# Kernel optimization log

Hardware: AMD Instinct MI355X
Metric: run time of the kernel (lower is better)

## Reference

```python
import jax, jax.numpy as jnp
import numpy as np

N_NODES = 100000
N_EDGES = 1600000
IN, HID, OUT = 32, 32, 16


def setup_inputs() -> dict:
    key = jax.random.key(0)
    ks = jax.random.split(key, 8)
    return {
        "features": jax.random.normal(ks[0], (N_NODES, IN), dtype=jnp.float32),
        "src": jax.random.randint(ks[1], (N_EDGES,), 0, N_NODES, dtype=jnp.int32),
        "dst": jax.random.randint(ks[2], (N_EDGES,), 0, N_NODES, dtype=jnp.int32),
        "edge_weight": jax.random.uniform(ks[3], (N_EDGES,), dtype=jnp.float32),
        "W1": jax.random.normal(ks[4], (IN, HID), dtype=jnp.float32) * 0.1,
        "b1": jnp.zeros((HID,), dtype=jnp.float32),
        "W2": jax.random.normal(ks[5], (HID, OUT), dtype=jnp.float32) * 0.1,
        "b2": jnp.zeros((OUT,), dtype=jnp.float32),
    }


def _graph_conv(h, W, b, src, dst, edge_weight, norm_src, norm_dst, n):
    # DGL GraphConv, norm='both', with edge_weight (u_mul_e aggregation)
    h = h * norm_src[:, None]          # out-degree^-0.5 on source side
    h = h @ W                          # dense transform (tiny GEMM)
    m = h[src] * edge_weight[:, None]  # gather + edge weighting  [E, d]
    agg = jax.ops.segment_sum(m, dst, num_segments=n)  # scatter-add SpMM
    return agg * norm_dst[:, None] + b # in-degree^-0.5 + bias


def reference(features, src, dst, edge_weight, W1, b1, W2, b2):
    n = features.shape[0]
    ones_e = jnp.ones_like(edge_weight)
    deg_out = jnp.clip(jax.ops.segment_sum(ones_e, src, num_segments=n), 1.0)
    deg_in = jnp.clip(jax.ops.segment_sum(ones_e, dst, num_segments=n), 1.0)
    norm_src = deg_out ** -0.5
    norm_dst = deg_in ** -0.5
    h = _graph_conv(features, W1, b1, src, dst, edge_weight, norm_src, norm_dst, n)
    h = jax.nn.relu(h)
    # dropout is identity in eval mode
    h = _graph_conv(h, W2, b2, src, dst, edge_weight, norm_src, norm_dst, n)
    return h
```

## Files before the change

### kernel.cpp

```cpp
#include <hip/hip_runtime.h>
#include <hip/hip_fp16.h>


#define NB   391
#define CAPB 5504
#define EPB  4096

__device__ __forceinline__ long nt_load_i64(const long* p) {
    return __builtin_nontemporal_load(p);
}

__global__ __launch_bounds__(1024) void partition_kernel(
        const int* __restrict__ src, const int* __restrict__ dst,
        const float* __restrict__ ew,
        int* __restrict__ g_cur_d, int* __restrict__ g_cur_s,
        int2* __restrict__ pack_part, unsigned char* __restrict__ src_part, int m) {
    __shared__ int hist_d[NB], hist_s[NB];
    __shared__ int lbase_d[NB], lbase_s[NB];
    __shared__ int gbase_d[NB], gbase_s[NB];
    __shared__ int cur_d[NB], cur_s[NB];
    __shared__ int woffd[16], woffs[16];
    __shared__ long stage[EPB];
    __shared__ unsigned short dbuck[EPB];
    __shared__ unsigned char  sstage[EPB];
    __shared__ unsigned short sbuck[EPB];
    int t = threadIdx.x, lane = t & 63, w = t >> 6;
    for (int i = t; i < NB; i += 1024) {
        hist_d[i] = 0; hist_s[i] = 0; cur_d[i] = 0; cur_s[i] = 0;
    }
    __syncthreads();
    int base_e = blockIdx.x * EPB;
    int total = m - base_e; if (total > EPB) total = EPB;
    int es[4], ed[4]; float wv[4];
#pragma unroll
    for (int k = 0; k < 4; k++) {
        int e = base_e + k * 1024 + t;
        if (e < m) { es[k] = src[e]; ed[k] = dst[e]; wv[k] = ew[e]; }
        else ed[k] = -1;
    }
#pragma unroll
    for (int k = 0; k < 4; k++) {
        if (ed[k] >= 0) {
            atomicAdd(&hist_d[ed[k] >> 8], 1);
            atomicAdd(&hist_s[es[k] >> 8], 1);
        }
    }
    __syncthreads();
    int hvd = (t < NB) ? hist_d[t] : 0;
    int hvs = (t < NB) ? hist_s[t] : 0;
    int vd = hvd, vs = hvs;
#pragma unroll
    for (int off = 1; off < 64; off <<= 1) {
        int ud = __shfl_up(vd, off, 64);
        int us = __shfl_up(vs, off, 64);
        if (lane >= off) { vd += ud; vs += us; }
    }
    if (lane == 63) { woffd[w] = vd; woffs[w] = vs; }
    __syncthreads();
    if (t < 64) {
        int sd = (t < 16) ? woffd[t] : 0;
        int ss = (t < 16) ? woffs[t] : 0;
        int od = sd, os = ss;
#pragma unroll
        for (int off = 1; off < 16; off <<= 1) {
            int ud = __shfl_up(sd, off, 64);
            int us = __shfl_up(ss, off, 64);
            if (lane >= off) { sd += ud; ss += us; }
        }
        if (t < 16) { woffd[t] = sd - od; woffs[t] = ss - os; }
    }
    __syncthreads();
    if (t < NB) {
        lbase_d[t] = vd + woffd[w] - hvd;
        lbase_s[t] = vs + woffs[w] - hvs;
    }
    for (int i = t; i < NB; i += 1024) {
        int c = hist_d[i];
        gbase_d[i] = i * CAPB + (c ? atomicAdd(&g_cur_d[i], c) : 0);
        c = hist_s[i];
        gbase_s[i] = i * CAPB + (c ? atomicAdd(&g_cur_s[i], c) : 0);
    }
    __syncthreads();
#pragma unroll
    for (int k = 0; k < 4; k++) {
        if (ed[k] >= 0) {
            int d = ed[k], s = es[k];
            int bd = d >> 8;
            int r = atomicAdd(&cur_d[bd], 1);
            int pos = lbase_d[bd] + r;
            stage[pos] = (long)(unsigned int)(s | ((d & 255) << 20)) |
                         ((long)__float_as_int(wv[k]) << 32);
            dbuck[pos] = (unsigned short)bd;
            int bs = s >> 8;
            int rs = atomicAdd(&cur_s[bs], 1);
            int ps = lbase_s[bs] + rs;
            sstage[ps] = (unsigned char)(s & 255);
            sbuck[ps] = (unsigned short)bs;
        }
    }
    __syncthreads();
    long* packl = (long*)pack_part;
    for (int i = t; i < total; i += 1024) {
        int b = dbuck[i];
        packl[(size_t)gbase_d[b] + (i - lbase_d[b])] = stage[i];
    }
    for (int i = t; i < total; i += 1024) {
        int b = sbuck[i];
        src_part[(size_t)gbase_s[b] + (i - lbase_s[b])] = sstage[i];
    }
}

__global__ __launch_bounds__(1024) void csr_kernel(
                           const int2* __restrict__ pack_part,
                           const unsigned char* __restrict__ src_part,
                           const int* __restrict__ g_cur_d, const int* __restrict__ g_cur_s,
                           const float* __restrict__ feat, const float* __restrict__ W1,
                           int2* __restrict__ csr, int2* __restrict__ rs_cnt,
                           float* __restrict__ norm_src, float* __restrict__ norm_dst,
                           __half* __restrict__ h1, int n) {
    __shared__ int cnt[256];
    __shared__ int rowx[256];
    __shared__ int cur[256];
    __shared__ int cnt_s[256];
    __shared__ float nsrc[256];
    __shared__ float sW1[1024];
    extern __shared__ int2 stage[];
    int t = threadIdx.x, b = blockIdx.x;
    if (t < 256) { cnt[t] = 0; cur[t] = 0; cnt_s[t] = 0; }
    sW1[t] = W1[t];
    __syncthreads();
    int count = g_cur_d[b]; if (count > CAPB) count = CAPB;
    int count_s = g_cur_s[b]; if (count_s > CAPB) count_s = CAPB;
    const int2* p = pack_part + (size_t)b * CAPB;
    const unsigned char* sp = src_part + (size_t)b * CAPB;
    int2 pk[4];
#pragma unroll
    for (int u = 0; u < 4; u++) {
        int e = t + u * 1024;
        if (e < count) { pk[u] = p[e]; atomicAdd(&cnt[pk[u].x >> 20], 1); }
    }
    for (int e = t + 4096; e < count; e += 1024)
        atomicAdd(&cnt[p[e].x >> 20], 1);
    for (int e = t; e < count_s; e += 1024) atomicAdd(&cnt_s[sp[e]], 1);
    __syncthreads();
    if (t < 256) {
        int node = b * 256 + t;
        if (node < n) {
            int cs = cnt_s[t];
            float ns = rsqrtf((float)(cs > 1 ? cs : 1));
            nsrc[t] = ns;
            norm_src[node] = ns;
        } else nsrc[t] = 0.0f;
    }
    if (t < 64) {
        int c0 = cnt[t * 4], c1 = cnt[t * 4 + 1], c2 = cnt[t * 4 + 2], c3 = cnt[t * 4 + 3];
        int tot = c0 + c1 + c2 + c3;
        int incl = tot;
#pragma unroll
        for (int off = 1; off < 64; off <<= 1) {
            int u = __shfl_up(incl, off, 64);
            if (t >= off) incl += u;
        }
        int excl = incl - tot;
        rowx[t * 4]     = excl;
        rowx[t * 4 + 1] = excl + c0;
        rowx[t * 4 + 2] = excl + c0 + c1;
        rowx[t * 4 + 3] = excl + c0 + c1 + c2;
    }
    __syncthreads();
    if (t < 256) {
        int node = b * 256 + t;
        if (node < n) {
            rs_cnt[node] = make_int2(b * CAPB + rowx[t], cnt[t]);
            norm_dst[node] = rsqrtf((float)(cnt[t] > 1 ? cnt[t] : 1));
        }
    }
    __syncthreads();
#pragma unroll
    for (int u = 0; u < 4; u++) {
        int e = t + u * 1024;
        if (e < count) {
            int2 v = pk[u];
            int dl = v.x >> 20;
            int r = atomicAdd(&cur[dl], 1);
            stage[rowx[dl] + r] = make_int2(v.x & 0x1FFFF, v.y);
        }
    }
    for (int e = t + 4096; e < count; e += 1024) {
        int2 v = p[e];
        int dl = v.x >> 20;
        int r = atomicAdd(&cur[dl], 1);
        stage[rowx[dl] + r] = make_int2(v.x & 0x1FFFF, v.y);
    }
    __syncthreads();
    int2* outp = csr + (size_t)b * CAPB;
    for (int e = t; e < count; e += 1024) outp[e] = stage[e];
    __syncthreads();
    float* sF = (float*)stage;
    int node0 = b * 256;
    int lim = n - node0; if (lim > 256) lim = 256; if (lim < 0) lim = 0;
    for (int o = t; o < lim * 32; o += 1024) {
        int i = o >> 5, k = o & 31;
        sF[o] = feat[(size_t)(node0 + i) * 32 + k] * nsrc[i];
    }
    __syncthreads();
    for (int o = t; o < lim * 32; o += 1024) {
        int i = o >> 5, col = o & 31;
        float acc = 0.0f;
#pragma unroll
        for (int k = 0; k < 32; k++) acc += sF[i * 32 + k] * sW1[k * 32 + col];
        h1[(size_t)(node0 + i) * 32 + col] = __float2half(acc);
    }
}

__global__ void gather1_fused_kernel(const __half* __restrict__ h1, const int2* __restrict__ csr,
                                     const int2* __restrict__ rs_cnt,
                                     const float* __restrict__ norm_src, const float* __restrict__ norm_dst,
                                     const float* __restrict__ W2, const float* __restrict__ b1,
                                     __half* __restrict__ h2, int n) {
    __shared__ float sW2[32 * 16];
    __shared__ float sB1[32];
    __shared__ float sX[4][8][33];
    int t = threadIdx.x;
    for (int i = t; i < 512; i += 256) sW2[i] = W2[i];
    if (t < 32) sB1[t] = b1[t];
    __syncthreads();
    int w = t >> 6, lane = t & 63;
    int q = lane >> 3;
    int dq = lane & 7;
    int node = (blockIdx.x * 4 + w) * 8 + q;
    bool valid = node < n;
    int2 rc = valid ? rs_cnt[node] : make_int2(0, 0);
    long base = rc.x;
    int c = rc.y;
    const float2* tv = (const float2*)h1;
    const long* csrl = (const long*)csr;
    float a00=0,a01=0,a02=0,a03=0, a10=0,a11=0,a12=0,a13=0;
    float a20=0,a21=0,a22=0,a23=0, a30=0,a31=0,a32=0,a33=0;
    int j = 0;
    for (; j + 3 < c; j += 4) {
        long q0 = nt_load_i64(csrl + base + j);
        long q1 = nt_load_i64(csrl + base + j + 1);
        long q2 = nt_load_i64(csrl + base + j + 2);
        long q3 = nt_load_i64(csrl + base + j + 3);
        float2 r0 = tv[(size_t)((int)q0 & 0xFFFFF) * 8 + dq];
        float2 r1 = tv[(size_t)((int)q1 & 0xFFFFF) * 8 + dq];
        float2 r2 = tv[(size_t)((int)q2 & 0xFFFFF) * 8 + dq];
        float2 r3 = tv[(size_t)((int)q3 & 0xFFFFF) * 8 + dq];
        float w0 = __int_as_float((int)(q0 >> 32)), w1 = __int_as_float((int)(q1 >> 32));
        float w2 = __int_as_float((int)(q2 >> 32)), w3 = __int_as_float((int)(q3 >> 32));
        float2 l0 = __half22float2(*(__half2*)&r0.x), h0 = __half22float2(*(__half2*)&r0.y);
        float2 l1 = __half22float2(*(__half2*)&r1.x), h1v = __half22float2(*(__half2*)&r1.y);
        float2 l2 = __half22float2(*(__half2*)&r2.x), h2v = __half22float2(*(__half2*)&r2.y);
        float2 l3 = __half22float2(*(__half2*)&r3.x), h3v = __half22float2(*(__half2*)&r3.y);
        a00 += l0.x * w0; a01 += l0.y * w0; a02 += h0.x * w0; a03 += h0.y * w0;
        a10 += l1.x * w1; a11 += l1.y * w1; a12 += h1v.x * w1; a13 += h1v.y * w1;
        a20 += l2.x * w2; a21 += l2.y * w2; a22 += h2v.x * w2; a23 += h2v.y * w2;
        a30 += l3.x * w3; a31 += l3.y * w3; a32 += h3v.x * w3; a33 += h3v.y * w3;
    }
    for (; j < c; j++) {
        long qq = nt_load_i64(csrl + base + j);
        float2 r = tv[(size_t)((int)qq & 0xFFFFF) * 8 + dq];
        float ww = __int_as_float((int)(qq >> 32));
        float2 l = __half22float2(*(__half2*)&r.x), h = __half22float2(*(__half2*)&r.y);
        a00 += l.x * ww; a01 += l.y * ww; a02 += h.x * ww; a03 += h.y * ww;
    }
    float s0 = (a00 + a10) + (a20 + a30);
    float s1 = (a01 + a11) + (a21 + a31);
    float s2 = (a02 + a12) + (a22 + a32);
    float s3 = (a03 + a13) + (a23 + a33);
    if (valid) {
        float nd = norm_dst[node], ns = norm_src[node];
        int d0 = 4 * dq;
        sX[w][q][d0]     = fmaxf(s0 * nd + sB1[d0],     0.0f) * ns;
        sX[w][q][d0 + 1] = fmaxf(s1 * nd + sB1[d0 + 1], 0.0f) * ns;
        sX[w][q][d0 + 2] = fmaxf(s2 * nd + sB1[d0 + 2], 0.0f) * ns;
        sX[w][q][d0 + 3] = fmaxf(s3 * nd + sB1[d0 + 3], 0.0f) * ns;
    }
    if (valid) {
        float o0 = 0.0f, o1 = 0.0f;
        int c0 = 2 * dq, c1 = 2 * dq + 1;
#pragma unroll
        for (int k = 0; k < 32; k++) {
            float x = sX[w][q][k];
            o0 += x * sW2[k * 16 + c0];
            o1 += x * sW2[k * 16 + c1];
        }
        ((__half2*)h2)[(size_t)node * 8 + dq] = __floats2half2_rn(o0, o1);
    }
}

__global__ void gather2_kernel(const __half* __restrict__ h2, const int2* __restrict__ csr,
                               const int2* __restrict__ rs_cnt,
                               const float* __restrict__ norm_dst, const float* __restrict__ b2,
                               float* __restrict__ out, int n) {
    int t = threadIdx.x;
    int w = t >> 6, lane = t & 63;
    int q = lane >> 2;
    int dq = lane & 3;
    int node = (blockIdx.x * 4 + w) * 16 + q;
    bool valid = node < n;
    int2 rc = valid ? rs_cnt[node] : make_int2(0, 0);
    long base = rc.x;
    int c = rc.y;
    const float2* tv = (const float2*)h2;
    const long* csrl = (const long*)csr;
    float a00=0,a01=0,a02=0,a03=0, a10=0,a11=0,a12=0,a13=0;
    float a20=0,a21=0,a22=0,a23=0, a30=0,a31=0,a32=0,a33=0;
    int j = 0;
    for (; j + 3 < c; j += 4) {
        long q0 = nt_load_i64(csrl + base + j);
        long q1 = nt_load_i64(csrl + base + j + 1);
        long q2 = nt_load_i64(csrl + base + j + 2);
        long q3 = nt_load_i64(csrl + base + j + 3);
        float2 r0 = tv[(size_t)((int)q0 & 0xFFFFF) * 4 + dq];
        float2 r1 = tv[(size_t)((int)q1 & 0xFFFFF) * 4 + dq];
        float2 r2 = tv[(size_t)((int)q2 & 0xFFFFF) * 4 + dq];
        float2 r3 = tv[(size_t)((int)q3 & 0xFFFFF) * 4 + dq];
        float w0 = __int_as_float((int)(q0 >> 32)), w1 = __int_as_float((int)(q1 >> 32));
        float w2 = __int_as_float((int)(q2 >> 32)), w3 = __int_as_float((int)(q3 >> 32));
        float2 l0 = __half22float2(*(__half2*)&r0.x), h0 = __half22float2(*(__half2*)&r0.y);
        float2 l1 = __half22float2(*(__half2*)&r1.x), h1v = __half22float2(*(__half2*)&r1.y);
        float2 l2 = __half22float2(*(__half2*)&r2.x), h2v = __half22float2(*(__half2*)&r2.y);
        float2 l3 = __half22float2(*(__half2*)&r3.x), h3v = __half22float2(*(__half2*)&r3.y);
        a00 += l0.x * w0; a01 += l0.y * w0; a02 += h0.x * w0; a03 += h0.y * w0;
        a10 += l1.x * w1; a11 += l1.y * w1; a12 += h1v.x * w1; a13 += h1v.y * w1;
        a20 += l2.x * w2; a21 += l2.y * w2; a22 += h2v.x * w2; a23 += h2v.y * w2;
        a30 += l3.x * w3; a31 += l3.y * w3; a32 += h3v.x * w3; a33 += h3v.y * w3;
    }
    for (; j < c; j++) {
        long qq = nt_load_i64(csrl + base + j);
        float2 r = tv[(size_t)((int)qq & 0xFFFFF) * 4 + dq];
        float ww = __int_as_float((int)(qq >> 32));
        float2 l = __half22float2(*(__half2*)&r.x), h = __half22float2(*(__half2*)&r.y);
        a00 += l.x * ww; a01 += l.y * ww; a02 += h.x * ww; a03 += h.y * ww;
    }
    if (valid) {
        float nd = norm_dst[node];
        int d0 = 4 * dq;
        float4 o;
        o.x = ((a00 + a10) + (a20 + a30)) * nd + b2[d0];
        o.y = ((a01 + a11) + (a21 + a31)) * nd + b2[d0 + 1];
        o.z = ((a02 + a12) + (a22 + a32)) * nd + b2[d0 + 2];
        o.w = ((a03 + a13) + (a23 + a33)) * nd + b2[d0 + 3];
        ((float4*)out)[(size_t)node * 4 + dq] = o;
    }
}

extern "C" void kernel_launch(void* const* d_in, const int* in_sizes, int n_in,
                              void* d_out, int out_size, void* d_ws, size_t ws_size,
                              hipStream_t stream) {
    const float* feat = (const float*)d_in[0];
    const int*   src  = (const int*)d_in[1];
    const int*   dst  = (const int*)d_in[2];
    const float* ew   = (const float*)d_in[3];
    const float* W1   = (const float*)d_in[4];
    const float* b1   = (const float*)d_in[5];
    const float* W2   = (const float*)d_in[6];
    const float* b2   = (const float*)d_in[7];
    float* out = (float*)d_out;

    const int n = in_sizes[0] / 32;
    const int m = in_sizes[1];

    char* wsb = (char*)d_ws;
    int2*   pack_part = (int2*)wsb;
    int2*   csr       = pack_part + (size_t)NB * CAPB;
    __half* h1        = (__half*)(csr + (size_t)NB * CAPB);
    __half* h2        = h1 + 32 * (size_t)n;
    float*  norm_src  = (float*)(h2 + 16 * (size_t)n);
    float*  norm_dst  = norm_src + n;
    int2*   rs_cnt    = (int2*)(norm_dst + n);
    int*    g_cur_d   = (int*)(rs_cnt + n);
    int*    g_cur_s   = g_cur_d + NB;
    unsigned char* src_part = (unsigned char*)(g_cur_s + NB);

    hipMemsetAsync(g_cur_d, 0, 2 * NB * sizeof(int), stream);

    partition_kernel<<<(m + EPB - 1) / EPB, 1024, 0, stream>>>(src, dst, ew, g_cur_d, g_cur_s,
                                                               pack_part, src_part, m);
    csr_kernel<<<NB, 1024, CAPB * sizeof(int2), stream>>>(pack_part, src_part, g_cur_d, g_cur_s,
                                                          feat, W1, csr, rs_cnt,
                                                          norm_src, norm_dst, h1, n);
    gather1_fused_kernel<<<(n + 31) / 32, 256, 0, stream>>>(h1, csr, rs_cnt,
                                                            norm_src, norm_dst, W2, b1, h2, n);
    gather2_kernel<<<(n + 63) / 64, 256, 0, stream>>>(h2, csr, rs_cnt, norm_dst, b2, out, n);
}
```

Before: 186.8 us.

## Sub-sort CSR rows by source range to improve gather locality

The CSR build now buckets each destination row's edges into four sub-buckets keyed on the source node's high bits. This uses a 1024-entry histogram and scan instead of 256. Per-node sub-counts are stored so the first gather kernel walks the four source-range segments in order, aiming for better cache locality on the h1 feature gathers. It costs more shared-memory atomics and scan work in csr_kernel, plus an extra per-node ushort4 array and shorter inner loops with more tail iterations in gather1.

```diff
diff --git a/kernel.cpp b/kernel.cpp
--- a/kernel.cpp
+++ b/kernel.cpp
@@ -116,17 +116,19 @@
                            const int* __restrict__ g_cur_d, const int* __restrict__ g_cur_s,
                            const float* __restrict__ feat, const float* __restrict__ W1,
                            int2* __restrict__ csr, int2* __restrict__ rs_cnt,
+                           ushort4* __restrict__ subcnt,
                            float* __restrict__ norm_src, float* __restrict__ norm_dst,
                            __half* __restrict__ h1, int n) {
-    __shared__ int cnt[256];
-    __shared__ int rowx[256];
-    __shared__ int cur[256];
+    __shared__ int cnt4[1024];
+    __shared__ int rowx4[1024];
+    __shared__ int cur4[1024];
     __shared__ int cnt_s[256];
     __shared__ float nsrc[256];
     __shared__ float sW1[1024];
     extern __shared__ int2 stage[];
     int t = threadIdx.x, b = blockIdx.x;
-    if (t < 256) { cnt[t] = 0; cur[t] = 0; cnt_s[t] = 0; }
+    cnt4[t] = 0; cur4[t] = 0;
+    if (t < 256) cnt_s[t] = 0;
     sW1[t] = W1[t];
     __syncthreads();
     int count = g_cur_d[b]; if (count > CAPB) count = CAPB;
@@ -137,10 +139,16 @@
 #pragma unroll
     for (int u = 0; u < 4; u++) {
         int e = t + u * 1024;
-        if (e < count) { pk[u] = p[e]; atomicAdd(&cnt[pk[u].x >> 20], 1); }
-    }
-    for (int e = t + 4096; e < count; e += 1024)
-        atomicAdd(&cnt[p[e].x >> 20], 1);
+        if (e < count) {
+            pk[u] = p[e];
+            int key = ((pk[u].x >> 20) << 2) | ((pk[u].x & 0x1FFFF) >> 15);
+            atomicAdd(&cnt4[key], 1);
+        }
+    }
+    for (int e = t + 4096; e < count; e += 1024) {
+        int2 v = p[e];
+        atomicAdd(&cnt4[((v.x >> 20) << 2) | ((v.x & 0x1FFFF) >> 15)], 1);
+    }
     for (int e = t; e < count_s; e += 1024) atomicAdd(&cnt_s[sp[e]], 1);
     __syncthreads();
     if (t < 256) {
@@ -153,26 +161,30 @@
         } else nsrc[t] = 0.0f;
     }
     if (t < 64) {
-        int c0 = cnt[t * 4], c1 = cnt[t * 4 + 1], c2 = cnt[t * 4 + 2], c3 = cnt[t * 4 + 3];
-        int tot = c0 + c1 + c2 + c3;
-        int incl = tot;
+        int base16 = t * 16;
+        int loc[16]; int sum = 0;
+#pragma unroll
+        for (int i = 0; i < 16; i++) { loc[i] = cnt4[base16 + i]; sum += loc[i]; }
+        int incl = sum;
 #pragma unroll
         for (int off = 1; off < 64; off <<= 1) {
             int u = __shfl_up(incl, off, 64);
             if (t >= off) incl += u;
         }
-        int excl = incl - tot;
-        rowx[t * 4]     = excl;
-        rowx[t * 4 + 1] = excl + c0;
-        rowx[t * 4 + 2] = excl + c0 + c1;
-        rowx[t * 4 + 3] = excl + c0 + c1 + c2;
+        int run = incl - sum;
+#pragma unroll
+        for (int i = 0; i < 16; i++) { rowx4[base16 + i] = run; run += loc[i]; }
     }
     __syncthreads();
     if (t < 256) {
+        int c0 = cnt4[4 * t], c1 = cnt4[4 * t + 1], c2 = cnt4[4 * t + 2], c3 = cnt4[4 * t + 3];
+        int tot = c0 + c1 + c2 + c3;
         int node = b * 256 + t;
         if (node < n) {
-            rs_cnt[node] = make_int2(b * CAPB + rowx[t], cnt[t]);
-            norm_dst[node] = rsqrtf((float)(cnt[t] > 1 ? cnt[t] : 1));
+            rs_cnt[node] = make_int2(b * CAPB + rowx4[4 * t], tot);
+            norm_dst[node] = rsqrtf((float)(tot > 1 ? tot : 1));
+            subcnt[node] = make_ushort4((unsigned short)c0, (unsigned short)c1,
+                                        (unsigned short)c2, (unsigned short)c3);
         }
     }
     __syncthreads();
@@ -181,16 +193,16 @@
         int e = t + u * 1024;
         if (e < count) {
             int2 v = pk[u];
-            int dl = v.x >> 20;
-            int r = atomicAdd(&cur[dl], 1);
-            stage[rowx[dl] + r] = make_int2(v.x & 0x1FFFF, v.y);
+            int key = ((v.x >> 20) << 2) | ((v.x & 0x1FFFF) >> 15);
+            int r = atomicAdd(&cur4[key], 1);
+            stage[rowx4[key] + r] = make_int2(v.x & 0x1FFFF, v.y);
         }
     }
     for (int e = t + 4096; e < count; e += 1024) {
         int2 v = p[e];
-        int dl = v.x >> 20;
-        int r = atomicAdd(&cur[dl], 1);
-        stage[rowx[dl] + r] = make_int2(v.x & 0x1FFFF, v.y);
+        int key = ((v.x >> 20) << 2) | ((v.x & 0x1FFFF) >> 15);
+        int r = atomicAdd(&cur4[key], 1);
+        stage[rowx4[key] + r] = make_int2(v.x & 0x1FFFF, v.y);
     }
     __syncthreads();
     int2* outp = csr + (size_t)b * CAPB;
@@ -215,6 +227,7 @@
 
 __global__ void gather1_fused_kernel(const __half* __restrict__ h1, const int2* __restrict__ csr,
                                      const int2* __restrict__ rs_cnt,
+                                     const ushort4* __restrict__ subcnt,
                                      const float* __restrict__ norm_src, const float* __restrict__ norm_dst,
                                      const float* __restrict__ W2, const float* __restrict__ b1,
                                      __half* __restrict__ h2, int n) {
@@ -231,39 +244,45 @@
     int node = (blockIdx.x * 4 + w) * 8 + q;
     bool valid = node < n;
     int2 rc = valid ? rs_cnt[node] : make_int2(0, 0);
-    long base = rc.x;
-    int c = rc.y;
+    ushort4 sc = valid ? subcnt[node] : make_ushort4(0, 0, 0, 0);
     const float2* tv = (const float2*)h1;
     const long* csrl = (const long*)csr;
     float a00=0,a01=0,a02=0,a03=0, a10=0,a11=0,a12=0,a13=0;
     float a20=0,a21=0,a22=0,a23=0, a30=0,a31=0,a32=0,a33=0;
-    int j = 0;
-    for (; j + 3 < c; j += 4) {
-        long q0 = nt_load_i64(csrl + base + j);
-        long q1 = nt_load_i64(csrl + base + j + 1);
-        long q2 = nt_load_i64(csrl + base + j + 2);
-        long q3 = nt_load_i64(csrl + base + j + 3);
-        float2 r0 = tv[(size_t)((int)q0 & 0xFFFFF) * 8 + dq];
-        float2 r1 = tv[(size_t)((int)q1 & 0xFFFFF) * 8 + dq];
-        float2 r2 = tv[(size_t)((int)q2 & 0xFFFFF) * 8 + dq];
-        float2 r3 = tv[(size_t)((int)q3 & 0xFFFFF) * 8 + dq];
-        float w0 = __int_as_float((int)(q0 >> 32)), w1 = __int_as_float((int)(q1 >> 32));
-        float w2 = __int_as_float((int)(q2 >> 32)), w3 = __int_as_float((int)(q3 >> 32));
-        float2 l0 = __half22float2(*(__half2*)&r0.x), h0 = __half22float2(*(__half2*)&r0.y);
-        float2 l1 = __half22float2(*(__half2*)&r1.x), h1v = __half22float2(*(__half2*)&r1.y);
-        float2 l2 = __half22float2(*(__half2*)&r2.x), h2v = __half22float2(*(__half2*)&r2.y);
-        float2 l3 = __half22float2(*(__half2*)&r3.x), h3v = __half22float2(*(__half2*)&r3.y);
-        a00 += l0.x * w0; a01 += l0.y * w0; a02 += h0.x * w0; a03 += h0.y * w0;
-        a10 += l1.x * w1; a11 += l1.y * w1; a12 += h1v.x * w1; a13 += h1v.y * w1;
-        a20 += l2.x * w2; a21 += l2.y * w2; a22 += h2v.x * w2; a23 += h2v.y * w2;
-        a30 += l3.x * w3; a31 += l3.y * w3; a32 += h3v.x * w3; a33 += h3v.y * w3;
-    }
-    for (; j < c; j++) {
-        long qq = nt_load_i64(csrl + base + j);
-        float2 r = tv[(size_t)((int)qq & 0xFFFFF) * 8 + dq];
-        float ww = __int_as_float((int)(qq >> 32));
-        float2 l = __half22float2(*(__half2*)&r.x), h = __half22float2(*(__half2*)&r.y);
-        a00 += l.x * ww; a01 += l.y * ww; a02 += h.x * ww; a03 += h.y * ww;
+    int st = rc.x;
+#pragma unroll
+    for (int rr = 0; rr < 4; rr++) {
+        int c = (rr == 0) ? (int)sc.x : (rr == 1) ? (int)sc.y
+              : (rr == 2) ? (int)sc.z : (int)sc.w;
+        long base = st; st += c;
+        int j = 0;
+        for (; j + 3 < c; j += 4) {
+            long q0 = nt_load_i64(csrl + base + j);
+            long q1 = nt_load_i64(csrl + base + j + 1);
+            long q2 = nt_load_i64(csrl + base + j + 2);
+            long q3 = nt_load_i64(csrl + base + j + 3);
+            float2 r0 = tv[(size_t)((int)q0 & 0xFFFFF) * 8 + dq];
+            float2 r1 = tv[(size_t)((int)q1 & 0xFFFFF) * 8 + dq];
+            float2 r2 = tv[(size_t)((int)q2 & 0xFFFFF) * 8 + dq];
+            float2 r3 = tv[(size_t)((int)q3 & 0xFFFFF) * 8 + dq];
+            float w0 = __int_as_float((int)(q0 >> 32)), w1 = __int_as_float((int)(q1 >> 32));
+            float w2 = __int_as_float((int)(q2 >> 32)), w3 = __int_as_float((int)(q3 >> 32));
+            float2 l0 = __half22float2(*(__half2*)&r0.x), h0 = __half22float2(*(__half2*)&r0.y);
+            float2 l1 = __half22float2(*(__half2*)&r1.x), h1v = __half22float2(*(__half2*)&r1.y);
+            float2 l2 = __half22float2(*(__half2*)&r2.x), h2v = __half22float2(*(__half2*)&r2.y);
+            float2 l3 = __half22float2(*(__half2*)&r3.x), h3v = __half22float2(*(__half2*)&r3.y);
+            a00 += l0.x * w0; a01 += l0.y * w0; a02 += h0.x * w0; a03 += h0.y * w0;
+            a10 += l1.x * w1; a11 += l1.y * w1; a12 += h1v.x * w1; a13 += h1v.y * w1;
+            a20 += l2.x * w2; a21 += l2.y * w2; a22 += h2v.x * w2; a23 += h2v.y * w2;
+            a30 += l3.x * w3; a31 += l3.y * w3; a32 += h3v.x * w3; a33 += h3v.y * w3;
+        }
+        for (; j < c; j++) {
+            long qq = nt_load_i64(csrl + base + j);
+            float2 r = tv[(size_t)((int)qq & 0xFFFFF) * 8 + dq];
+            float ww = __int_as_float((int)(qq >> 32));
+            float2 l = __half22float2(*(__half2*)&r.x), h = __half22float2(*(__half2*)&r.y);
+            a00 += l.x * ww; a01 += l.y * ww; a02 += h.x * ww; a03 += h.y * ww;
+        }
     }
     float s0 = (a00 + a10) + (a20 + a30);
     float s1 = (a01 + a11) + (a21 + a31);
@@ -364,15 +383,16 @@
     const int m = in_sizes[1];
 
     char* wsb = (char*)d_ws;
-    int2*   pack_part = (int2*)wsb;
-    int2*   csr       = pack_part + (size_t)NB * CAPB;
-    __half* h1        = (__half*)(csr + (size_t)NB * CAPB);
-    __half* h2        = h1 + 32 * (size_t)n;
-    float*  norm_src  = (float*)(h2 + 16 * (size_t)n);
-    float*  norm_dst  = norm_src + n;
-    int2*   rs_cnt    = (int2*)(norm_dst + n);
-    int*    g_cur_d   = (int*)(rs_cnt + n);
-    int*    g_cur_s   = g_cur_d + NB;
+    int2*    pack_part = (int2*)wsb;
+    int2*    csr       = pack_part + (size_t)NB * CAPB;
+    __half*  h1        = (__half*)(csr + (size_t)NB * CAPB);
+    __half*  h2        = h1 + 32 * (size_t)n;
+    float*   norm_src  = (float*)(h2 + 16 * (size_t)n);
+    float*   norm_dst  = norm_src + n;
+    int2*    rs_cnt    = (int2*)(norm_dst + n);
+    ushort4* subcnt    = (ushort4*)(rs_cnt + n);
+    int*     g_cur_d   = (int*)(subcnt + n);
+    int*     g_cur_s   = g_cur_d + NB;
     unsigned char* src_part = (unsigned char*)(g_cur_s + NB);
 
     hipMemsetAsync(g_cur_d, 0, 2 * NB * sizeof(int), stream);
@@ -380,9 +400,9 @@
     partition_kernel<<<(m + EPB - 1) / EPB, 1024, 0, stream>>>(src, dst, ew, g_cur_d, g_cur_s,
                                                                pack_part, src_part, m);
     csr_kernel<<<NB, 1024, CAPB * sizeof(int2), stream>>>(pack_part, src_part, g_cur_d, g_cur_s,
-                                                          feat, W1, csr, rs_cnt,
+                                                          feat, W1, csr, rs_cnt, subcnt,
                                                           norm_src, norm_dst, h1, n);
-    gather1_fused_kernel<<<(n + 31) / 32, 256, 0, stream>>>(h1, csr, rs_cnt,
+    gather1_fused_kernel<<<(n + 31) / 32, 256, 0, stream>>>(h1, csr, rs_cnt, subcnt,
                                                             norm_src, norm_dst, W2, b1, h2, n);
     gather2_kernel<<<(n + 63) / 64, 256, 0, stream>>>(h2, csr, rs_cnt, norm_dst, b2, out, n);
 }
```

Result: slower. 194.4 us (+4.0%).

## Split first-layer gather into two feature-half passes to shrink gather footprint

Applied to the files above, without the earlier changes.

The 32-wide half-precision layer-1 features are stored as two separate 16-column arrays, and the layer-1 gather runs as two passes, one per half. Each pass does a partial second-layer GEMM. Pass 0 writes fp32 partials to a scratch buffer and pass 1 adds them and emits h2. The aim is to halve the random-gather working set per pass so it fits better in cache, at the cost of reading the CSR twice, an extra launch, and extra partial-sum traffic.

```diff
diff --git a/kernel.cpp b/kernel.cpp
--- a/kernel.cpp
+++ b/kernel.cpp
@@ -5,6 +5,8 @@
 #define NB   391
 #define CAPB 5504
 #define EPB  4096
+
+typedef float f32x4 __attribute__((ext_vector_type(4)));
 
 __device__ __forceinline__ long nt_load_i64(const long* p) {
     return __builtin_nontemporal_load(p);
@@ -117,7 +119,7 @@
                            const float* __restrict__ feat, const float* __restrict__ W1,
                            int2* __restrict__ csr, int2* __restrict__ rs_cnt,
                            float* __restrict__ norm_src, float* __restrict__ norm_dst,
-                           __half* __restrict__ h1, int n) {
+                           __half* __restrict__ h1a, __half* __restrict__ h1b, int n) {
     __shared__ int cnt[256];
     __shared__ int rowx[256];
     __shared__ int cur[256];
@@ -209,31 +211,34 @@
         float acc = 0.0f;
 #pragma unroll
         for (int k = 0; k < 32; k++) acc += sF[i * 32 + k] * sW1[k * 32 + col];
-        h1[(size_t)(node0 + i) * 32 + col] = __float2half(acc);
-    }
-}
-
-__global__ void gather1_fused_kernel(const __half* __restrict__ h1, const int2* __restrict__ csr,
-                                     const int2* __restrict__ rs_cnt,
-                                     const float* __restrict__ norm_src, const float* __restrict__ norm_dst,
-                                     const float* __restrict__ W2, const float* __restrict__ b1,
-                                     __half* __restrict__ h2, int n) {
-    __shared__ float sW2[32 * 16];
-    __shared__ float sB1[32];
-    __shared__ float sX[4][8][33];
+        __half hv = __float2half(acc);
+        if (col < 16) h1a[(size_t)(node0 + i) * 16 + col]        = hv;
+        else          h1b[(size_t)(node0 + i) * 16 + (col - 16)] = hv;
+    }
+}
+
+template<int PASS>
+__global__ void gather1_pass(const __half* __restrict__ h1x, const int2* __restrict__ csr,
+                             const int2* __restrict__ rs_cnt,
+                             const float* __restrict__ norm_src, const float* __restrict__ norm_dst,
+                             const float* __restrict__ W2, const float* __restrict__ b1,
+                             float* __restrict__ part, __half* __restrict__ h2, int n) {
+    __shared__ float sW2h[256];
+    __shared__ float sB[16];
+    __shared__ float sX[4][16][17];
     int t = threadIdx.x;
-    for (int i = t; i < 512; i += 256) sW2[i] = W2[i];
-    if (t < 32) sB1[t] = b1[t];
+    if (t < 256) sW2h[t] = W2[PASS * 256 + t];
+    if (t < 16)  sB[t] = b1[PASS * 16 + t];
     __syncthreads();
     int w = t >> 6, lane = t & 63;
-    int q = lane >> 3;
-    int dq = lane & 7;
-    int node = (blockIdx.x * 4 + w) * 8 + q;
+    int q = lane >> 2;
+    int dq = lane & 3;
+    int node = (blockIdx.x * 4 + w) * 16 + q;
     bool valid = node < n;
     int2 rc = valid ? rs_cnt[node] : make_int2(0, 0);
     long base = rc.x;
     int c = rc.y;
-    const float2* tv = (const float2*)h1;
+    const float2* tv = (const float2*)h1x;
     const long* csrl = (const long*)csr;
     float a00=0,a01=0,a02=0,a03=0, a10=0,a11=0,a12=0,a13=0;
     float a20=0,a21=0,a22=0,a23=0, a30=0,a31=0,a32=0,a33=0;
@@ -243,10 +248,10 @@
         long q1 = nt_load_i64(csrl + base + j + 1);
         long q2 = nt_load_i64(csrl + base + j + 2);
         long q3 = nt_load_i64(csrl + base + j + 3);
-        float2 r0 = tv[(size_t)((int)q0 & 0xFFFFF) * 8 + dq];
-        float2 r1 = tv[(size_t)((int)q1 & 0xFFFFF) * 8 + dq];
-        float2 r2 = tv[(size_t)((int)q2 & 0xFFFFF) * 8 + dq];
-        float2 r3 = tv[(size_t)((int)q3 & 0xFFFFF) * 8 + dq];
+        float2 r0 = tv[(size_t)((int)q0 & 0xFFFFF) * 4 + dq];
+        float2 r1 = tv[(size_t)((int)q1 & 0xFFFFF) * 4 + dq];
+        float2 r2 = tv[(size_t)((int)q2 & 0xFFFFF) * 4 + dq];
+        float2 r3 = tv[(size_t)((int)q3 & 0xFFFFF) * 4 + dq];
         float w0 = __int_as_float((int)(q0 >> 32)), w1 = __int_as_float((int)(q1 >> 32));
         float w2 = __int_as_float((int)(q2 >> 32)), w3 = __int_as_float((int)(q3 >> 32));
         float2 l0 = __half22float2(*(__half2*)&r0.x), h0 = __half22float2(*(__half2*)&r0.y);
@@ -260,7 +265,7 @@
     }
     for (; j < c; j++) {
         long qq = nt_load_i64(csrl + base + j);
-        float2 r = tv[(size_t)((int)qq & 0xFFFFF) * 8 + dq];
+        float2 r = tv[(size_t)((int)qq & 0xFFFFF) * 4 + dq];
         float ww = __int_as_float((int)(qq >> 32));
         float2 l = __half22float2(*(__half2*)&r.x), h = __half22float2(*(__half2*)&r.y);
         a00 += l.x * ww; a01 += l.y * ww; a02 += h.x * ww; a03 += h.y * ww;
@@ -272,21 +277,35 @@
     if (valid) {
         float nd = norm_dst[node], ns = norm_src[node];
         int d0 = 4 * dq;
-        sX[w][q][d0]     = fmaxf(s0 * nd + sB1[d0],     0.0f) * ns;
-        sX[w][q][d0 + 1] = fmaxf(s1 * nd + sB1[d0 + 1], 0.0f) * ns;
-        sX[w][q][d0 + 2] = fmaxf(s2 * nd + sB1[d0 + 2], 0.0f) * ns;
-        sX[w][q][d0 + 3] = fmaxf(s3 * nd + sB1[d0 + 3], 0.0f) * ns;
+        sX[w][q][d0]     = fmaxf(s0 * nd + sB[d0],     0.0f) * ns;
+        sX[w][q][d0 + 1] = fmaxf(s1 * nd + sB[d0 + 1], 0.0f) * ns;
+        sX[w][q][d0 + 2] = fmaxf(s2 * nd + sB[d0 + 2], 0.0f) * ns;
+        sX[w][q][d0 + 3] = fmaxf(s3 * nd + sB[d0 + 3], 0.0f) * ns;
     }
     if (valid) {
-        float o0 = 0.0f, o1 = 0.0f;
-        int c0 = 2 * dq, c1 = 2 * dq + 1;
-#pragma unroll
-        for (int k = 0; k < 32; k++) {
+        float o0 = 0.0f, o1 = 0.0f, o2 = 0.0f, o3 = 0.0f;
+        int c0 = 4 * dq;
+#pragma unroll
+        for (int k = 0; k < 16; k++) {
             float x = sX[w][q][k];
-            o0 += x * sW2[k * 16 + c0];
-            o1 += x * sW2[k * 16 + c1];
-        }
-        ((__half2*)h2)[(size_t)node * 8 + dq] = __floats2half2_rn(o0, o1);
+            o0 += x * sW2h[k * 16 + c0];
+            o1 += x * sW2h[k * 16 + c0 + 1];
+            o2 += x * sW2h[k * 16 + c0 + 2];
+            o3 += x * sW2h[k * 16 + c0 + 3];
+        }
+        if (PASS == 0) {
+            f32x4 pv = { o0, o1, o2, o3 };
+            __builtin_nontemporal_store(pv, (f32x4*)part + (size_t)node * 4 + dq);
+        } else {
+            f32x4 pv = __builtin_nontemporal_load((const f32x4*)part + (size_t)node * 4 + dq);
+            o0 += pv.x; o1 += pv.y; o2 += pv.z; o3 += pv.w;
+            __half2 lo = __floats2half2_rn(o0, o1);
+            __half2 hi = __floats2half2_rn(o2, o3);
+            float2 st;
+            st.x = __uint_as_float(*(unsigned int*)&lo);
+            st.y = __uint_as_float(*(unsigned int*)&hi);
+            ((float2*)h2)[(size_t)node * 4 + dq] = st;
+        }
     }
 }
 
@@ -366,9 +385,11 @@
     char* wsb = (char*)d_ws;
     int2*   pack_part = (int2*)wsb;
     int2*   csr       = pack_part + (size_t)NB * CAPB;
-    __half* h1        = (__half*)(csr + (size_t)NB * CAPB);
-    __half* h2        = h1 + 32 * (size_t)n;
-    float*  norm_src  = (float*)(h2 + 16 * (size_t)n);
+    __half* h1a       = (__half*)(csr + (size_t)NB * CAPB);
+    __half* h1b       = h1a + 16 * (size_t)n;
+    __half* h2        = h1b + 16 * (size_t)n;
+    float*  part      = (float*)(h2 + 16 * (size_t)n);
+    float*  norm_src  = part + 16 * (size_t)n;
     float*  norm_dst  = norm_src + n;
     int2*   rs_cnt    = (int2*)(norm_dst + n);
     int*    g_cur_d   = (int*)(rs_cnt + n);
@@ -381,8 +402,11 @@
                                                                pack_part, src_part, m);
     csr_kernel<<<NB, 1024, CAPB * sizeof(int2), stream>>>(pack_part, src_part, g_cur_d, g_cur_s,
                                                           feat, W1, csr, rs_cnt,
-                                                          norm_src, norm_dst, h1, n);
-    gather1_fused_kernel<<<(n + 31) / 32, 256, 0, stream>>>(h1, csr, rs_cnt,
-                                                            norm_src, norm_dst, W2, b1, h2, n);
+                                                          norm_src, norm_dst, h1a, h1b, n);
+    int g1grid = (n + 63) / 64;
+    gather1_pass<0><<<g1grid, 256, 0, stream>>>(h1a, csr, rs_cnt, norm_src, norm_dst,
+                                                W2, b1, part, h2, n);
+    gather1_pass<1><<<g1grid, 256, 0, stream>>>(h1b, csr, rs_cnt, norm_src, norm_dst,
+                                                W2, b1, part, h2, n);
     gather2_kernel<<<(n + 63) / 64, 256, 0, stream>>>(h2, csr, rs_cnt, norm_dst, b2, out, n);
 }
```

Measured after the change: 209.5 us. +12.1%, slower.
